# Performance work log

Hardware: AMD Instinct MI355X
Metric: run time of the kernel (lower is better)

The kernel has to match this reference:

```python
import jax, jax.numpy as jnp
import numpy as np

VOCAB, D, L, H, B, S = 10000, 512, 6, 8, 32, 384
DK = D // H
DFF = 4 * D
EPS = 1e-5


def setup_inputs() -> dict:
    key = jax.random.key(0)
    ks = jax.random.split(key, 24)
    sc = 0.02
    emb = jax.random.normal(ks[0], (VOCAB, D), jnp.float32) * sc
    emb = emb.at[0].set(0.0)  # padding_idx=0
    inp = {
        'input_id': jax.random.randint(ks[1], (B, S), 0, VOCAB),
        'intensity': jax.random.uniform(ks[2], (B, 1, S), jnp.float32),
        'emb': emb,
        'iw': jax.random.normal(ks[3], (1, D), jnp.float32) * sc,
        'ib': jnp.zeros((D,), jnp.float32),
        'Wq': jax.random.normal(ks[4], (L, D, D), jnp.float32) * sc,
        'bq': jnp.zeros((L, D), jnp.float32),
        'Wk': jax.random.normal(ks[5], (L, D, D), jnp.float32) * sc,
        'bk': jnp.zeros((L, D), jnp.float32),
        'Wv': jax.random.normal(ks[6], (L, D, D), jnp.float32) * sc,
        'bv': jnp.zeros((L, D), jnp.float32),
        'Wo': jax.random.normal(ks[7], (L, D, D), jnp.float32) * sc,
        'bo': jnp.zeros((L, D), jnp.float32),
        'ln1w': jnp.ones((L, D), jnp.float32),
        'ln1b': jnp.zeros((L, D), jnp.float32),
        'ln2w': jnp.ones((L, D), jnp.float32),
        'ln2b': jnp.zeros((L, D), jnp.float32),
        'W1': jax.random.normal(ks[8], (L, D, DFF), jnp.float32) * sc,
        'b1': jnp.zeros((L, DFF), jnp.float32),
        'W2': jax.random.normal(ks[9], (L, DFF, D), jnp.float32) * sc,
        'b2': jnp.zeros((L, D), jnp.float32),
    }
    return inp


def _ln(x, w, b):
    m = jnp.mean(x, axis=-1, keepdims=True)
    v = jnp.mean((x - m) ** 2, axis=-1, keepdims=True)
    return (x - m) / jnp.sqrt(v + EPS) * w + b


def _block(x, pad_mask, Wq, bq, Wk, bk, Wv, bv, Wo, bo, ln1w, ln1b, ln2w, ln2b, W1, b1, W2, b2):
    b, s, d = x.shape
    h = _ln(x, ln1w, ln1b)
    q = (h @ Wq + bq).reshape(b, s, H, DK).transpose(0, 2, 1, 3)  # [B,H,S,DK]
    k = (h @ Wk + bk).reshape(b, s, H, DK).transpose(0, 2, 1, 3)
    v = (h @ Wv + bv).reshape(b, s, H, DK).transpose(0, 2, 1, 3)
    scores = jnp.einsum('bhqd,bhkd->bhqk', q, k) / jnp.sqrt(jnp.float32(DK))
    scores = jnp.where(pad_mask, -1e9, scores)  # mask keys at pad positions
    p = jax.nn.softmax(scores, axis=-1)
    attn = jnp.einsum('bhqk,bhkd->bhqd', p, v)
    attn = attn.transpose(0, 2, 1, 3).reshape(b, s, d)
    x = x + (attn @ Wo + bo)
    h2 = _ln(x, ln2w, ln2b)
    ffn = jax.nn.gelu(h2 @ W1 + b1, approximate=False) @ W2 + b2
    return x + ffn


def reference(input_id, intensity, emb, iw, ib, Wq, bq, Wk, bk, Wv, bv, Wo, bo,
              ln1w, ln1b, ln2w, ln2b, W1, b1, W2, b2):
    # predict() path of MSBERT (deterministic; training forward adds random masking)
    inten = jnp.swapaxes(intensity, 1, 2) @ iw + ib          # [B,S,D]
    x = emb[input_id] + inten                                 # token emb + intensity proj
    pad_mask = (input_id == 0)[:, None, None, :]              # [B,1,1,S] broadcast over queries
    for i in range(L):
        x = _block(x, pad_mask, Wq[i], bq[i], Wk[i], bk[i], Wv[i], bv[i], Wo[i], bo[i],
                   ln1w[i], ln1b[i], ln2w[i], ln2b[i], W1[i], b1[i], W2[i], b2[i])
    pool = jnp.matmul(intensity, x) / jnp.float32(intensity.shape[1])  # [B,1,D]
    return pool
```

## Files before the change

kernel.cpp:

```cpp
#include <hip/hip_runtime.h>
#include <math.h>

#define VOCAB 10000
#define D 512
#define L 6
#define H 8
#define B 32
#define S 384
#define DK 64
#define DFF 2048
#define TOK (B * S)
#define TD ((size_t)TOK * D)

typedef unsigned short u16;
using bf16x8 = __attribute__((ext_vector_type(8))) short;
using f32x4  = __attribute__((ext_vector_type(4))) float;
using u16x4  = __attribute__((ext_vector_type(4))) unsigned short;

__device__ u16   g_x[TD];
__device__ u16   g_h[TD];
__device__ u16   g_q[TD];
__device__ u16   g_k[TD];
__device__ u16   g_vt[TD];
__device__ u16   g_ffn[(size_t)TOK * DFF];
__device__ u16   g_qkvT[(size_t)L * 3 * D * D];
__device__ u16   g_woT[(size_t)L * D * D];
__device__ u16   g_w1T[(size_t)L * DFF * D];
__device__ u16   g_w2T[(size_t)L * D * DFF];
__device__ float g_bqkv[L * 3 * D];
__device__ float g_pool[B * 6 * D];

__device__ __forceinline__ u16 f2bf(float f) {
  unsigned int u = __builtin_bit_cast(unsigned int, f);
  u = (u + 0x7fffu + ((u >> 16) & 1u)) >> 16;
  return (u16)u;
}
__device__ __forceinline__ float bf2f(u16 v) {
  unsigned int u = ((unsigned int)v) << 16;
  return __builtin_bit_cast(float, u);
}

__device__ __forceinline__ void gld16(const void* g, void* l) {
  __builtin_amdgcn_global_load_lds(
      (const __attribute__((address_space(1))) unsigned int*)g,
      (__attribute__((address_space(3))) unsigned int*)l, 16, 0, 0);
}

__global__ __launch_bounds__(256) void embed_kernel(
    const int* __restrict__ ids, const float* __restrict__ inten,
    const float* __restrict__ emb, const float* __restrict__ iw,
    const float* __restrict__ ib, u16* __restrict__ x) {
  int tok = blockIdx.x;
  int t = threadIdx.x;
  int id = ids[tok];
  float it = inten[tok];
  const float* er = emb + (size_t)id * D;
  u16* xr = x + (size_t)tok * D;
  xr[t]       = f2bf(er[t] + it * iw[t] + ib[t]);
  xr[t + 256] = f2bf(er[t + 256] + it * iw[t + 256] + ib[t + 256]);
}

__global__ __launch_bounds__(256) void ln_kernel(
    const u16* __restrict__ x, const float* __restrict__ w,
    const float* __restrict__ b, u16* __restrict__ out) {
  int tok = blockIdx.x * 4 + (threadIdx.x >> 6);
  int lane = threadIdx.x & 63;
  const u16* xr = x + (size_t)tok * D + lane * 8;
  bf16x8 v8 = *(const bf16x8*)xr;
  float v[8];
  float s = 0.f, ss = 0.f;
  #pragma unroll
  for (int i = 0; i < 8; ++i) {
    v[i] = bf2f((u16)v8[i]);
    s += v[i];
    ss += v[i] * v[i];
  }
  #pragma unroll
  for (int o = 1; o < 64; o <<= 1) {
    s += __shfl_xor(s, o);
    ss += __shfl_xor(ss, o);
  }
  float mean = s * (1.0f / (float)D);
  float var = ss * (1.0f / (float)D) - mean * mean;
  float rstd = rsqrtf(var + 1e-5f);
  float4 w0 = *(const float4*)(w + lane * 8);
  float4 w1 = *(const float4*)(w + lane * 8 + 4);
  float4 b0 = *(const float4*)(b + lane * 8);
  float4 b1 = *(const float4*)(b + lane * 8 + 4);
  float wv[8] = {w0.x, w0.y, w0.z, w0.w, w1.x, w1.y, w1.z, w1.w};
  float bv[8] = {b0.x, b0.y, b0.z, b0.w, b1.x, b1.y, b1.z, b1.w};
  bf16x8 o8;
  #pragma unroll
  for (int i = 0; i < 8; ++i)
    o8[i] = (short)f2bf((v[i] - mean) * rstd * wv[i] + bv[i]);
  *(bf16x8*)(out + (size_t)tok * D + lane * 8) = o8;
}

__global__ __launch_bounds__(256) void transpose_cvt(
    const float* __restrict__ src, u16* __restrict__ dst,
    int K, int N, size_t sstride, size_t dstride) {
  __shared__ float tile[32][33];
  int n0 = blockIdx.x * 32, k0 = blockIdx.y * 32, l = blockIdx.z;
  src += (size_t)l * sstride;
  dst += (size_t)l * dstride;
  int tx = threadIdx.x & 31, ty = threadIdx.x >> 5;
  #pragma unroll
  for (int i = 0; i < 32; i += 8)
    tile[ty + i][tx] = src[(size_t)(k0 + ty + i) * N + n0 + tx];
  __syncthreads();
  #pragma unroll
  for (int i = 0; i < 32; i += 8)
    dst[(size_t)(n0 + ty + i) * K + k0 + tx] = f2bf(tile[tx][ty + i]);
}

__global__ __launch_bounds__(256) void transpose_qkvo(
    const float* __restrict__ Wq, const float* __restrict__ Wk,
    const float* __restrict__ Wv, const float* __restrict__ Wo,
    u16* __restrict__ qkvT, u16* __restrict__ woT) {
  __shared__ float tile[32][33];
  int z = blockIdx.z;
  int l = z >> 2, which = z & 3;
  const float* src = (which == 0 ? Wq : which == 1 ? Wk : which == 2 ? Wv : Wo)
                     + (size_t)l * D * D;
  u16* dst = (which < 3) ? (qkvT + (size_t)l * 3 * D * D + (size_t)which * D * D)
                         : (woT + (size_t)l * D * D);
  int n0 = blockIdx.x * 32, k0 = blockIdx.y * 32;
  int tx = threadIdx.x & 31, ty = threadIdx.x >> 5;
  #pragma unroll
  for (int i = 0; i < 32; i += 8)
    tile[ty + i][tx] = src[(size_t)(k0 + ty + i) * D + n0 + tx];
  __syncthreads();
  #pragma unroll
  for (int i = 0; i < 32; i += 8)
    dst[(size_t)(n0 + ty + i) * D + k0 + tx] = f2bf(tile[tx][ty + i]);
}

__global__ __launch_bounds__(256) void concat_bias(
    const float* __restrict__ bq, const float* __restrict__ bk,
    const float* __restrict__ bv, float* __restrict__ dst) {
  int i = blockIdx.x * 256 + threadIdx.x;
  int l = i / 1536, c = i % 1536;
  float v = (c < 512) ? bq[l * 512 + c]
          : (c < 1024) ? bk[l * 512 + c - 512]
                       : bv[l * 512 + c - 1024];
  dst[i] = v;
}

template <int EPI>
__global__ __launch_bounds__(256) void mfma_gemm(
    const u16* __restrict__ A, const u16* __restrict__ Bt,
    const float* __restrict__ bias,
    u16* __restrict__ Oq, u16* __restrict__ Ok, u16* __restrict__ Ovt,
    int M, int N, int K) {
  __shared__ u16 As[2][128 * 32];
  __shared__ u16 Bs[2][128 * 32];
  int t = threadIdx.x;
  int lane = t & 63, w = t >> 6;
  int wr = w >> 1, wc = w & 1;

  int gm = gridDim.y, gn = gridDim.x;
  int wgid = blockIdx.y * gn + blockIdx.x;
  int xcd = wgid & 7;
  int c = wgid >> 3;
  int rpx = gm >> 3;
  int cg = c / gn;
  int bm = (xcd * rpx + cg) * 128;
  int bn = (c - cg * gn) * 128;

  int l15 = lane & 15, l4 = lane >> 4;

  int gswu = ((t & 3) ^ ((t >> 3) & 3)) * 8;
  const u16* a0 = A + (size_t)(bm + (t >> 2)) * K + gswu;
  const u16* a1 = A + (size_t)(bm + 64 + (t >> 2)) * K + gswu;
  const u16* b0 = Bt + (size_t)(bn + (t >> 2)) * K + gswu;
  const u16* b1 = Bt + (size_t)(bn + 64 + (t >> 2)) * K + gswu;
  unsigned off0 = (unsigned)(t & 192) * 16u;
  unsigned off1 = off0 + 256u * 16u;
  int rxu = (l4 ^ ((l15 >> 1) & 3)) * 8;

  f32x4 acc[4][4];
  #pragma unroll
  for (int mi = 0; mi < 4; ++mi)
    #pragma unroll
    for (int nj = 0; nj < 4; ++nj)
      acc[mi][nj] = f32x4{0.f, 0.f, 0.f, 0.f};

  int nt = K >> 5;

#define STAGE_T(ti, bi) do { int k0s = (ti) * 32;            \
    gld16(a0 + k0s, (char*)As[bi] + off0);                   \
    gld16(a1 + k0s, (char*)As[bi] + off1);                   \
    gld16(b0 + k0s, (char*)Bs[bi] + off0);                   \
    gld16(b1 + k0s, (char*)Bs[bi] + off1); } while (0)

  STAGE_T(0, 0);
  STAGE_T(1, 1);

  for (int tt = 0; tt < nt; ++tt) {
    if (tt < nt - 1) asm volatile("s_waitcnt vmcnt(4)" ::: "memory");
    else             asm volatile("s_waitcnt vmcnt(0)" ::: "memory");
    __builtin_amdgcn_s_barrier();
    __builtin_amdgcn_sched_barrier(0);
    const u16* Asb = As[tt & 1];
    const u16* Bsb = Bs[tt & 1];
    bf16x8 af[4], bfr[4];
    #pragma unroll
    for (int mi = 0; mi < 4; ++mi)
      af[mi] = *(const bf16x8*)(Asb + (wr * 64 + mi * 16 + l15) * 32 + rxu);
    #pragma unroll
    for (int nj = 0; nj < 4; ++nj)
      bfr[nj] = *(const bf16x8*)(Bsb + (wc * 64 + nj * 16 + l15) * 32 + rxu);
    #pragma unroll
    for (int mi = 0; mi < 4; ++mi)
      #pragma unroll
      for (int nj = 0; nj < 4; ++nj)
        acc[mi][nj] = __builtin_amdgcn_mfma_f32_16x16x32_bf16(af[mi], bfr[nj], acc[mi][nj], 0, 0, 0);
    __builtin_amdgcn_sched_barrier(0);
    __builtin_amdgcn_s_barrier();
    if (tt + 2 < nt) STAGE_T(tt + 2, tt & 1);
  }
#undef STAGE_T

  int row00 = bm + wr * 64, col0 = bn + wc * 64;
  #pragma unroll
  for (int mi = 0; mi < 4; ++mi) {
    int rowb = row00 + mi * 16 + l4 * 4;
    #pragma unroll
    for (int nj = 0; nj < 4; ++nj) {
      int col = col0 + nj * 16 + l15;
      float bcol = bias[col];
      if (EPI == 0) {
        if (col < 512) {
          #pragma unroll
          for (int r = 0; r < 4; ++r)
            Oq[(size_t)(rowb + r) * D + col] = f2bf(acc[mi][nj][r] + bcol);
        } else if (col < 1024) {
          #pragma unroll
          for (int r = 0; r < 4; ++r)
            Ok[(size_t)(rowb + r) * D + (col - 512)] = f2bf(acc[mi][nj][r] + bcol);
        } else {
          int cv = col - 1024;
          int hh = cv >> 6, dk = cv & 63;
          int bb = rowb / S, ss = rowb - bb * S;
          u16x4 pk;
          #pragma unroll
          for (int r = 0; r < 4; ++r) pk[r] = f2bf(acc[mi][nj][r] + bcol);
          *(u16x4*)(Ovt + ((size_t)(bb * H + hh) * DK + dk) * S + ss) = pk;
        }
      } else {
        #pragma unroll
        for (int r = 0; r < 4; ++r) {
          float v = acc[mi][nj][r] + bcol;
          v = 0.5f * v * (1.0f + erff(v * 0.70710678118654752f));
          Oq[(size_t)(rowb + r) * N + col] = f2bf(v);
        }
      }
    }
  }
}

__global__ __launch_bounds__(256) void gemm64(
    const u16* __restrict__ A, const u16* __restrict__ Bt,
    const float* __restrict__ bias, u16* __restrict__ Cres,
    int M, int N, int K) {
  __shared__ u16 As[2][64 * 32];
  __shared__ u16 Bs[2][128 * 32];
  int t = threadIdx.x;
  int lane = t & 63, w = t >> 6;
  int wr = w >> 1, wc = w & 1;

  int gm = gridDim.y, gn = gridDim.x;
  int wgid = blockIdx.y * gn + blockIdx.x;
  int xcd = wgid & 7;
  int c = wgid >> 3;
  int rpx = gm >> 3;
  int cg = c / gn;
  int bm = (xcd * rpx + cg) * 64;
  int bn = (c - cg * gn) * 128;

  int l15 = lane & 15, l4 = lane >> 4;

  int arow = t >> 2, ag = t & 3;
  int aswu = (ag ^ ((arow >> 1) & 3)) * 8;
  const u16* a0 = A + (size_t)(bm + arow) * K + aswu;
  const u16* b0 = Bt + (size_t)(bn + arow) * K + aswu;
  const u16* b1 = Bt + (size_t)(bn + 64 + arow) * K + aswu;
  unsigned offA  = (unsigned)(w * 1024);
  unsigned offB0 = (unsigned)(w * 1024);
  unsigned offB1 = offB0 + 4096u;
  int rxu = (l4 ^ ((l15 >> 1) & 3)) * 8;

  f32x4 acc[2][4];
  #pragma unroll
  for (int mi = 0; mi < 2; ++mi)
    #pragma unroll
    for (int nj = 0; nj < 4; ++nj)
      acc[mi][nj] = f32x4{0.f, 0.f, 0.f, 0.f};

  int nt = K >> 5;

#define STG64(ti, bi) do { int k0s = (ti) * 32;              \
    gld16(a0 + k0s, (char*)As[bi] + offA);                   \
    gld16(b0 + k0s, (char*)Bs[bi] + offB0);                  \
    gld16(b1 + k0s, (char*)Bs[bi] + offB1); } while (0)

  STG64(0, 0);
  STG64(1, 1);

  for (int tt = 0; tt < nt; ++tt) {
    if (tt < nt - 1) asm volatile("s_waitcnt vmcnt(3)" ::: "memory");
    else             asm volatile("s_waitcnt vmcnt(0)" ::: "memory");
    __builtin_amdgcn_s_barrier();
    __builtin_amdgcn_sched_barrier(0);
    const u16* Asb = As[tt & 1];
    const u16* Bsb = Bs[tt & 1];
    bf16x8 af[2], bfr[4];
    #pragma unroll
    for (int mi = 0; mi < 2; ++mi)
      af[mi] = *(const bf16x8*)(Asb + (wr * 32 + mi * 16 + l15) * 32 + rxu);
    #pragma unroll
    for (int nj = 0; nj < 4; ++nj)
      bfr[nj] = *(const bf16x8*)(Bsb + (wc * 64 + nj * 16 + l15) * 32 + rxu);
    #pragma unroll
    for (int mi = 0; mi < 2; ++mi)
      #pragma unroll
      for (int nj = 0; nj < 4; ++nj)
        acc[mi][nj] = __builtin_amdgcn_mfma_f32_16x16x32_bf16(af[mi], bfr[nj], acc[mi][nj], 0, 0, 0);
    __builtin_amdgcn_sched_barrier(0);
    __builtin_amdgcn_s_barrier();
    if (tt + 2 < nt) STG64(tt + 2, tt & 1);
  }
#undef STG64

  int row00 = bm + wr * 32, col0 = bn + wc * 64;
  #pragma unroll
  for (int mi = 0; mi < 2; ++mi) {
    int rowb = row00 + mi * 16 + l4 * 4;
    #pragma unroll
    for (int nj = 0; nj < 4; ++nj) {
      int col = col0 + nj * 16 + l15;
      float bcol = bias[col];
      #pragma unroll
      for (int r = 0; r < 4; ++r) {
        size_t ci = (size_t)(rowb + r) * N + col;
        Cres[ci] = f2bf(bf2f(Cres[ci]) + acc[mi][nj][r] + bcol);
      }
    }
  }
}

__global__ __launch_bounds__(256) void attn_mfma(
    const u16* __restrict__ q, const u16* __restrict__ k,
    const u16* __restrict__ vt, const int* __restrict__ ids,
    u16* __restrict__ out) {
  __shared__ u16 Ks[64][72];
  __shared__ u16 Vs[64][72];
  __shared__ u16 Ps[4][32][72];
  __shared__ float Msall[S];
  int t = threadIdx.x, lane = t & 63, w = t >> 6;
  int l15 = lane & 15, l4 = lane >> 4;
  int bh = blockIdx.x;
  int b = bh >> 3, hh = bh & 7;
  int q0 = blockIdx.y * 128 + w * 32;

  for (int i = t; i < S; i += 256)
    Msall[i] = (ids[b * S + i] == 0) ? -1e9f : -8.0f;

  bf16x8 qf[2][2];
  const u16* qbase = q + (size_t)(b * S + q0) * D + hh * DK;
  #pragma unroll
  for (int mi = 0; mi < 2; ++mi)
    #pragma unroll
    for (int ks = 0; ks < 2; ++ks)
      qf[mi][ks] = *(const bf16x8*)(qbase + (size_t)(mi * 16 + l15) * D + ks * 32 + l4 * 8);

  int rr0 = t >> 3, ch0 = t & 7;
  int rr1 = (256 + t) >> 3, ch1 = t & 7;
  const size_t kbase = (size_t)(b * S) * D + hh * DK;
  const size_t vbase = (size_t)(b * H + hh) * DK * S;

  bf16x8 kr0, kr1, vr0, vr1;
  kr0 = *(const bf16x8*)(k + kbase + (size_t)rr0 * D + ch0 * 8);
  kr1 = *(const bf16x8*)(k + kbase + (size_t)rr1 * D + ch1 * 8);
  vr0 = *(const bf16x8*)(vt + vbase + (size_t)rr0 * S + 0 + ch0 * 8);
  vr1 = *(const bf16x8*)(vt + vbase + (size_t)rr1 * S + 0 + ch1 * 8);
  *(bf16x8*)(&Ks[rr0][ch0 * 8]) = kr0;
  *(bf16x8*)(&Ks[rr1][ch1 * 8]) = kr1;
  *(bf16x8*)(&Vs[rr0][ch0 * 8]) = vr0;
  *(bf16x8*)(&Vs[rr1][ch1 * 8]) = vr1;
  __syncthreads();

  float lsum[8];
  f32x4 accO[2][4];
  #pragma unroll
  for (int i = 0; i < 8; ++i) lsum[i] = 0.f;
  #pragma unroll
  for (int mi = 0; mi < 2; ++mi)
    #pragma unroll
    for (int nj = 0; nj < 4; ++nj)
      accO[mi][nj] = f32x4{0.f, 0.f, 0.f, 0.f};

  for (int kb = 0; kb < S; kb += 64) {
    bool more = (kb + 64) < S;
    if (more) {
      kr0 = *(const bf16x8*)(k + kbase + (size_t)(kb + 64 + rr0) * D + ch0 * 8);
      kr1 = *(const bf16x8*)(k + kbase + (size_t)(kb + 64 + rr1) * D + ch1 * 8);
      vr0 = *(const bf16x8*)(vt + vbase + (size_t)rr0 * S + kb + 64 + ch0 * 8);
      vr1 = *(const bf16x8*)(vt + vbase + (size_t)rr1 * S + kb + 64 + ch1 * 8);
    }

    f32x4 sc[2][4];
    #pragma unroll
    for (int mi = 0; mi < 2; ++mi)
      #pragma unroll
      for (int nj = 0; nj < 4; ++nj)
        sc[mi][nj] = f32x4{0.f, 0.f, 0.f, 0.f};
    __builtin_amdgcn_s_setprio(1);
    #pragma unroll
    for (int ks = 0; ks < 2; ++ks) {
      bf16x8 kf[4];
      #pragma unroll
      for (int nj = 0; nj < 4; ++nj)
        kf[nj] = *(const bf16x8*)(&Ks[nj * 16 + l15][ks * 32 + l4 * 8]);
      #pragma unroll
      for (int mi = 0; mi < 2; ++mi)
        #pragma unroll
        for (int nj = 0; nj < 4; ++nj)
          sc[mi][nj] = __builtin_amdgcn_mfma_f32_16x16x32_bf16(qf[mi][ks], kf[nj], sc[mi][nj], 0, 0, 0);
    }
    __builtin_amdgcn_s_setprio(0);
    #pragma unroll
    for (int mi = 0; mi < 2; ++mi)
      #pragma unroll
      for (int nj = 0; nj < 4; ++nj) {
        float mv = Msall[kb + nj * 16 + l15];
        #pragma unroll
        for (int r = 0; r < 4; ++r)
          sc[mi][nj][r] = __expf(sc[mi][nj][r] * 0.125f + mv);
      }
    #pragma unroll
    for (int mi = 0; mi < 2; ++mi)
      #pragma unroll
      for (int r = 0; r < 4; ++r) {
        float rs = sc[mi][0][r] + sc[mi][1][r] + sc[mi][2][r] + sc[mi][3][r];
        #pragma unroll
        for (int o = 1; o < 16; o <<= 1) rs += __shfl_xor(rs, o);
        lsum[mi * 4 + r] += rs;
      }
    #pragma unroll
    for (int mi = 0; mi < 2; ++mi)
      #pragma unroll
      for (int nj = 0; nj < 4; ++nj)
        #pragma unroll
        for (int r = 0; r < 4; ++r)
          Ps[w][mi * 16 + l4 * 4 + r][nj * 16 + l15] = f2bf(sc[mi][nj][r]);
    __builtin_amdgcn_s_setprio(1);
    #pragma unroll
    for (int ks2 = 0; ks2 < 2; ++ks2) {
      bf16x8 pf[2], vf[4];
      #pragma unroll
      for (int mi = 0; mi < 2; ++mi)
        pf[mi] = *(const bf16x8*)(&Ps[w][mi * 16 + l15][ks2 * 32 + l4 * 8]);
      #pragma unroll
      for (int nj = 0; nj < 4; ++nj)
        vf[nj] = *(const bf16x8*)(&Vs[nj * 16 + l15][ks2 * 32 + l4 * 8]);
      #pragma unroll
      for (int mi = 0; mi < 2; ++mi)
        #pragma unroll
        for (int nj = 0; nj < 4; ++nj)
          accO[mi][nj] = __builtin_amdgcn_mfma_f32_16x16x32_bf16(pf[mi], vf[nj], accO[mi][nj], 0, 0, 0);
    }
    __builtin_amdgcn_s_setprio(0);

    if (more) {
      __syncthreads();
      *(bf16x8*)(&Ks[rr0][ch0 * 8]) = kr0;
      *(bf16x8*)(&Ks[rr1][ch1 * 8]) = kr1;
      *(bf16x8*)(&Vs[rr0][ch0 * 8]) = vr0;
      *(bf16x8*)(&Vs[rr1][ch1 * 8]) = vr1;
      __syncthreads();
    }
  }

  #pragma unroll
  for (int mi = 0; mi < 2; ++mi)
    #pragma unroll
    for (int nj = 0; nj < 4; ++nj)
      #pragma unroll
      for (int r = 0; r < 4; ++r) {
        int row = b * S + q0 + mi * 16 + l4 * 4 + r;
        out[(size_t)row * D + hh * DK + nj * 16 + l15] =
            f2bf(accO[mi][nj][r] / lsum[mi * 4 + r]);
      }
}

__global__ __launch_bounds__(512) void pool_part(
    const u16* __restrict__ x, const float* __restrict__ inten,
    float* __restrict__ part) {
  int b = blockIdx.x, cchunk = blockIdx.y;
  int d = threadIdx.x;
  int s0 = cchunk * 64;
  float acc = 0.f;
  for (int s = s0; s < s0 + 64; ++s)
    acc += inten[b * S + s] * bf2f(x[((size_t)b * S + s) * D + d]);
  part[((size_t)b * 6 + cchunk) * D + d] = acc;
}
__global__ __launch_bounds__(512) void pool_reduce(
    const float* __restrict__ part, float* __restrict__ out) {
  int b = blockIdx.x, d = threadIdx.x;
  float acc = 0.f;
  #pragma unroll
  for (int c = 0; c < 6; ++c) acc += part[((size_t)b * 6 + c) * D + d];
  out[b * D + d] = acc;
}

extern "C" void kernel_launch(void* const* d_in, const int* in_sizes, int n_in,
                              void* d_out, int out_size, void* d_ws, size_t ws_size,
                              hipStream_t stream) {
  const int* input_id    = (const int*)d_in[0];
  const float* intensity = (const float*)d_in[1];
  const float* emb = (const float*)d_in[2];
  const float* iw  = (const float*)d_in[3];
  const float* ib  = (const float*)d_in[4];
  const float* Wq  = (const float*)d_in[5];
  const float* bq  = (const float*)d_in[6];
  const float* Wk  = (const float*)d_in[7];
  const float* bk  = (const float*)d_in[8];
  const float* Wv  = (const float*)d_in[9];
  const float* bv  = (const float*)d_in[10];
  const float* Wo  = (const float*)d_in[11];
  const float* bo  = (const float*)d_in[12];
  const float* ln1w = (const float*)d_in[13];
  const float* ln1b = (const float*)d_in[14];
  const float* ln2w = (const float*)d_in[15];
  const float* ln2b = (const float*)d_in[16];
  const float* W1  = (const float*)d_in[17];
  const float* b1  = (const float*)d_in[18];
  const float* W2  = (const float*)d_in[19];
  const float* b2  = (const float*)d_in[20];
  float* outp = (float*)d_out;

  float *bqkv, *poolp;
  u16 *x, *h, *q, *k, *vt, *ffn, *qkvT, *woT, *w1T, *w2T;
  { void* p; hipGetSymbolAddress(&p, HIP_SYMBOL(g_x));    x    = (u16*)p; }
  { void* p; hipGetSymbolAddress(&p, HIP_SYMBOL(g_h));    h    = (u16*)p; }
  { void* p; hipGetSymbolAddress(&p, HIP_SYMBOL(g_q));    q    = (u16*)p; }
  { void* p; hipGetSymbolAddress(&p, HIP_SYMBOL(g_k));    k    = (u16*)p; }
  { void* p; hipGetSymbolAddress(&p, HIP_SYMBOL(g_vt));   vt   = (u16*)p; }
  { void* p; hipGetSymbolAddress(&p, HIP_SYMBOL(g_ffn));  ffn  = (u16*)p; }
  { void* p; hipGetSymbolAddress(&p, HIP_SYMBOL(g_qkvT)); qkvT = (u16*)p; }
  { void* p; hipGetSymbolAddress(&p, HIP_SYMBOL(g_woT));  woT  = (u16*)p; }
  { void* p; hipGetSymbolAddress(&p, HIP_SYMBOL(g_w1T));  w1T  = (u16*)p; }
  { void* p; hipGetSymbolAddress(&p, HIP_SYMBOL(g_w2T));  w2T  = (u16*)p; }
  { void* p; hipGetSymbolAddress(&p, HIP_SYMBOL(g_bqkv)); bqkv = (float*)p; }
  { void* p; hipGetSymbolAddress(&p, HIP_SYMBOL(g_pool)); poolp = (float*)p; }

  dim3 t256(256);
  transpose_qkvo<<<dim3(16, 16, 4 * L), t256, 0, stream>>>(Wq, Wk, Wv, Wo, qkvT, woT);
  transpose_cvt<<<dim3(64, 16, L), t256, 0, stream>>>(W1, w1T, D, DFF, (size_t)D * DFF, (size_t)D * DFF);
  transpose_cvt<<<dim3(16, 64, L), t256, 0, stream>>>(W2, w2T, DFF, D, (size_t)DFF * D, (size_t)DFF * D);
  concat_bias<<<L * 3 * D / 256, t256, 0, stream>>>(bq, bk, bv, bqkv);

  embed_kernel<<<TOK, t256, 0, stream>>>(input_id, intensity, emb, iw, ib, x);

  for (int l = 0; l < L; ++l) {
    const u16* qkvT_l = qkvT + (size_t)l * 3 * D * D;
    const u16* woT_l  = woT + (size_t)l * D * D;
    const u16* w1T_l  = w1T + (size_t)l * D * DFF;
    const u16* w2T_l  = w2T + (size_t)l * DFF * D;

    ln_kernel<<<TOK / 4, t256, 0, stream>>>(x, ln1w + (size_t)l * D, ln1b + (size_t)l * D, h);
    mfma_gemm<0><<<dim3(12, 96), t256, 0, stream>>>(h, qkvT_l, bqkv + l * 3 * D,
                                                    q, k, vt, TOK, 3 * D, D);
    attn_mfma<<<dim3(B * H, S / 128), t256, 0, stream>>>(q, k, vt, input_id, h);
    gemm64<<<dim3(4, 192), t256, 0, stream>>>(h, woT_l, bo + (size_t)l * D,
                                              x, TOK, D, D);
    ln_kernel<<<TOK / 4, t256, 0, stream>>>(x, ln2w + (size_t)l * D, ln2b + (size_t)l * D, h);
    mfma_gemm<2><<<dim3(16, 96), t256, 0, stream>>>(h, w1T_l, b1 + (size_t)l * DFF,
                                                    ffn, nullptr, nullptr, TOK, DFF, D);
    gemm64<<<dim3(4, 192), t256, 0, stream>>>(ffn, w2T_l, b2 + (size_t)l * D,
                                              x, TOK, D, DFF);
  }

  pool_part<<<dim3(B, 6), dim3(512), 0, stream>>>(x, intensity, poolp);
  pool_reduce<<<B, dim3(512), 0, stream>>>(poolp, outp);
}
```

Before: 1.201 ms.

## Compute transposed attention scores to drop per-tile row-sum shuffles

The QK^T MFMA is computed with operands swapped, so each lane holds scores for one query row across four keys. This lets the softmax denominator accumulate lane-locally, replacing the per-tile 16-lane shuffle reductions with a single cross-lane reduction at the end. P is written to shared memory as packed 4-element vectors instead of scalar stores, and the final normalisation uses a reciprocal multiply. It also adds a shuffle epilogue to redistribute row sums, and the 66-element row padding may create LDS bank conflicts.

```diff
diff --git a/kernel.cpp b/kernel.cpp
--- a/kernel.cpp
+++ b/kernel.cpp
@@ -355,7 +355,7 @@
     u16* __restrict__ out) {
   __shared__ u16 Ks[64][72];
   __shared__ u16 Vs[64][72];
-  __shared__ u16 Ps[4][32][72];
+  __shared__ u16 Pt[4][32][66];
   __shared__ float Msall[S];
   int t = threadIdx.x, lane = t & 63, w = t >> 6;
   int l15 = lane & 15, l4 = lane >> 4;
@@ -390,77 +390,70 @@
   *(bf16x8*)(&Vs[rr1][ch1 * 8]) = vr1;
   __syncthreads();
 
-  float lsum[8];
+  float lsum_sw[2] = {0.f, 0.f};
   f32x4 accO[2][4];
-  #pragma unroll
-  for (int i = 0; i < 8; ++i) lsum[i] = 0.f;
   #pragma unroll
   for (int mi = 0; mi < 2; ++mi)
     #pragma unroll
     for (int nj = 0; nj < 4; ++nj)
       accO[mi][nj] = f32x4{0.f, 0.f, 0.f, 0.f};
 
-  for (int kb = 0; kb < S; kb += 64) {
-    bool more = (kb + 64) < S;
+  for (int kt = 0; kt < S; kt += 64) {
+    bool more = (kt + 64) < S;
     if (more) {
-      kr0 = *(const bf16x8*)(k + kbase + (size_t)(kb + 64 + rr0) * D + ch0 * 8);
-      kr1 = *(const bf16x8*)(k + kbase + (size_t)(kb + 64 + rr1) * D + ch1 * 8);
-      vr0 = *(const bf16x8*)(vt + vbase + (size_t)rr0 * S + kb + 64 + ch0 * 8);
-      vr1 = *(const bf16x8*)(vt + vbase + (size_t)rr1 * S + kb + 64 + ch1 * 8);
-    }
-
-    f32x4 sc[2][4];
-    #pragma unroll
-    for (int mi = 0; mi < 2; ++mi)
-      #pragma unroll
-      for (int nj = 0; nj < 4; ++nj)
-        sc[mi][nj] = f32x4{0.f, 0.f, 0.f, 0.f};
+      kr0 = *(const bf16x8*)(k + kbase + (size_t)(kt + 64 + rr0) * D + ch0 * 8);
+      kr1 = *(const bf16x8*)(k + kbase + (size_t)(kt + 64 + rr1) * D + ch1 * 8);
+      vr0 = *(const bf16x8*)(vt + vbase + (size_t)rr0 * S + kt + 64 + ch0 * 8);
+      vr1 = *(const bf16x8*)(vt + vbase + (size_t)rr1 * S + kt + 64 + ch1 * 8);
+    }
+
+    f32x4 scT[4][2];
+    #pragma unroll
+    for (int kb = 0; kb < 4; ++kb)
+      #pragma unroll
+      for (int mi = 0; mi < 2; ++mi)
+        scT[kb][mi] = f32x4{0.f, 0.f, 0.f, 0.f};
     __builtin_amdgcn_s_setprio(1);
     #pragma unroll
     for (int ks = 0; ks < 2; ++ks) {
       bf16x8 kf[4];
       #pragma unroll
-      for (int nj = 0; nj < 4; ++nj)
-        kf[nj] = *(const bf16x8*)(&Ks[nj * 16 + l15][ks * 32 + l4 * 8]);
-      #pragma unroll
-      for (int mi = 0; mi < 2; ++mi)
+      for (int kb = 0; kb < 4; ++kb)
+        kf[kb] = *(const bf16x8*)(&Ks[kb * 16 + l15][ks * 32 + l4 * 8]);
+      #pragma unroll
+      for (int kb = 0; kb < 4; ++kb)
         #pragma unroll
-        for (int nj = 0; nj < 4; ++nj)
-          sc[mi][nj] = __builtin_amdgcn_mfma_f32_16x16x32_bf16(qf[mi][ks], kf[nj], sc[mi][nj], 0, 0, 0);
+        for (int mi = 0; mi < 2; ++mi)
+          scT[kb][mi] = __builtin_amdgcn_mfma_f32_16x16x32_bf16(kf[kb], qf[mi][ks], scT[kb][mi], 0, 0, 0);
     }
     __builtin_amdgcn_s_setprio(0);
-    #pragma unroll
-    for (int mi = 0; mi < 2; ++mi)
-      #pragma unroll
-      for (int nj = 0; nj < 4; ++nj) {
-        float mv = Msall[kb + nj * 16 + l15];
+
+    #pragma unroll
+    for (int kb = 0; kb < 4; ++kb) {
+      float mvv[4];
+      #pragma unroll
+      for (int r = 0; r < 4; ++r)
+        mvv[r] = Msall[kt + kb * 16 + l4 * 4 + r];
+      #pragma unroll
+      for (int mi = 0; mi < 2; ++mi) {
+        u16x4 pk;
         #pragma unroll
-        for (int r = 0; r < 4; ++r)
-          sc[mi][nj][r] = __expf(sc[mi][nj][r] * 0.125f + mv);
+        for (int r = 0; r < 4; ++r) {
+          float p = __expf(scT[kb][mi][r] * 0.125f + mvv[r]);
+          lsum_sw[mi] += p;
+          pk[r] = f2bf(p);
+        }
+        *(u16x4*)(&Pt[w][mi * 16 + l15][kb * 16 + l4 * 4]) = pk;
       }
-    #pragma unroll
-    for (int mi = 0; mi < 2; ++mi)
-      #pragma unroll
-      for (int r = 0; r < 4; ++r) {
-        float rs = sc[mi][0][r] + sc[mi][1][r] + sc[mi][2][r] + sc[mi][3][r];
-        #pragma unroll
-        for (int o = 1; o < 16; o <<= 1) rs += __shfl_xor(rs, o);
-        lsum[mi * 4 + r] += rs;
-      }
-    #pragma unroll
-    for (int mi = 0; mi < 2; ++mi)
-      #pragma unroll
-      for (int nj = 0; nj < 4; ++nj)
-        #pragma unroll
-        for (int r = 0; r < 4; ++r)
-          Ps[w][mi * 16 + l4 * 4 + r][nj * 16 + l15] = f2bf(sc[mi][nj][r]);
+    }
+
     __builtin_amdgcn_s_setprio(1);
     #pragma unroll
     for (int ks2 = 0; ks2 < 2; ++ks2) {
       bf16x8 pf[2], vf[4];
       #pragma unroll
       for (int mi = 0; mi < 2; ++mi)
-        pf[mi] = *(const bf16x8*)(&Ps[w][mi * 16 + l15][ks2 * 32 + l4 * 8]);
+        pf[mi] = *(const bf16x8*)(&Pt[w][mi * 16 + l15][ks2 * 32 + l4 * 8]);
       #pragma unroll
       for (int nj = 0; nj < 4; ++nj)
         vf[nj] = *(const bf16x8*)(&Vs[nj * 16 + l15][ks2 * 32 + l4 * 8]);
@@ -482,6 +475,17 @@
     }
   }
 
+  float inv_[2][4];
+  #pragma unroll
+  for (int mi = 0; mi < 2; ++mi) {
+    float tot = lsum_sw[mi];
+    tot += __shfl_xor(tot, 16);
+    tot += __shfl_xor(tot, 32);
+    #pragma unroll
+    for (int r = 0; r < 4; ++r)
+      inv_[mi][r] = 1.0f / __shfl(tot, l4 * 4 + r);
+  }
+
   #pragma unroll
   for (int mi = 0; mi < 2; ++mi)
     #pragma unroll
@@ -490,7 +494,7 @@
       for (int r = 0; r < 4; ++r) {
         int row = b * S + q0 + mi * 16 + l4 * 4 + r;
         out[(size_t)row * D + hh * DK + nj * 16 + l15] =
-            f2bf(accO[mi][nj][r] / lsum[mi * 4 + r]);
+            f2bf(accO[mi][nj][r] * inv_[mi][r]);
       }
 }
 
```

After: 1.157 ms, median of 2. -3.7%, faster.
